# Performance work log

Hardware: AMD Instinct MI355X
Metric: run time of the kernel (lower is better)

The kernel has to match this reference:

```python
import jax, jax.numpy as jnp
import numpy as np

SEQ, BATCH, IN_DIM, HID = 1024, 512, 128, 128


def _linear_params(key, fan_in, fan_out):
    # matches torch nn.Linear default init: U(-1/sqrt(fan_in), 1/sqrt(fan_in))
    s = 1.0 / np.sqrt(fan_in)
    k1, k2 = jax.random.split(key)
    W = jax.random.uniform(k1, (fan_in, fan_out), minval=-s, maxval=s, dtype=jnp.float32)
    b = jax.random.uniform(k2, (fan_out,), minval=-s, maxval=s, dtype=jnp.float32)
    return W, b


def setup_inputs() -> dict:
    key = jax.random.key(0)
    ks = jax.random.split(key, 5)
    inputs = jax.random.normal(ks[0], (SEQ, BATCH, IN_DIM), dtype=jnp.float32)
    Wf, bf = _linear_params(ks[1], IN_DIM + HID, HID)
    Wi, bi = _linear_params(ks[2], IN_DIM + HID, HID)
    Wg, bg = _linear_params(ks[3], IN_DIM + HID, HID)
    Wo, bo = _linear_params(ks[4], IN_DIM + HID, HID)
    return {"inputs": inputs, "Wf": Wf, "bf": bf, "Wi": Wi, "bi": bi,
            "Wg": Wg, "bg": bg, "Wo": Wo, "bo": bo}


def reference(inputs, Wf, bf, Wi, bi, Wg, bg, Wo, bo):
    # inputs: [seq, batch, in_dim] (time-major, matches torch unbind(dim=0))
    B = inputs.shape[1]
    H = Wf.shape[1]
    h0 = jnp.zeros((B, H), dtype=inputs.dtype)
    c0 = jnp.zeros((B, H), dtype=inputs.dtype)

    def step(carry, x):
        hx, cx = carry
        comb = jnp.concatenate([x, hx], axis=1)  # [B, in_dim+H]
        f_lin = comb @ Wf + bf
        i_lin = comb @ Wi + bi
        g = jnp.tanh(comb @ Wg + bg)
        o = jax.nn.sigmoid(comb @ Wo + bo)
        # Quantum sampler, closed form:
        #  - RX(theta)|0> has <Z> = cos(theta)
        #  - CNOT chain over f-wires pulls Z_j back to Z_0...Z_j -> cumprod of cos
        #  - i-wires untouched by CNOTs -> plain cos
        #  probs = (<Z> + 1) / 2
        f = (jnp.cumprod(jnp.cos(f_lin), axis=1) + 1.0) * 0.5
        i = (jnp.cos(i_lin) + 1.0) * 0.5
        cx_new = f * cx + i * g
        hx_new = o * jnp.tanh(cx_new)
        return (hx_new, cx_new), hx_new

    (hx, cx), outputs = jax.lax.scan(step, (h0, c0), inputs)
    return outputs, hx, cx
```

## Files before the change

kernel.cpp:

```cpp
#include <hip/hip_runtime.h>

#define SEQ   1024
#define BATCH 512
#define HID   128

typedef __attribute__((ext_vector_type(8))) short  short8v;
typedef __attribute__((ext_vector_type(4))) float  float4v;
typedef __attribute__((ext_vector_type(2))) float  float2v;

__device__ __forceinline__ unsigned short f2bf(float f) {
    union { float f; unsigned u; } v; v.f = f;
    return (unsigned short)((v.u + 0x7fffu + ((v.u >> 16) & 1u)) >> 16);
}
__device__ __forceinline__ float fast_cos(float x) {
    return __builtin_amdgcn_cosf(x * 0.15915494309189535f);
}
__device__ __forceinline__ float fast_sigmoid(float x) {
    return __builtin_amdgcn_rcpf(1.0f + __builtin_amdgcn_exp2f(-1.4426950408889634f * x));
}
__device__ __forceinline__ float fast_tanh(float x) {
    return 1.0f - 2.0f * __builtin_amdgcn_rcpf(1.0f + __builtin_amdgcn_exp2f(2.8853900817779268f * x));
}
template<int CTRL, int RM>
__device__ __forceinline__ float dpp1(float v) {
    union { float f; int i; } s, o, r;
    s.f = v; o.f = 1.0f;
    r.i = __builtin_amdgcn_update_dpp(o.i, s.i, CTRL, RM, 0xf, false);
    return r.f;
}
#define BAR() do { asm volatile("s_waitcnt lgkmcnt(0)" ::: "memory");  \
                   __builtin_amdgcn_s_barrier();                       \
                   __builtin_amdgcn_sched_barrier(0); } while (0)

__global__ __launch_bounds__(512, 1) void qlstm_fused(
    const float* __restrict__ X,
    const float* __restrict__ Wf, const float* __restrict__ bfp,
    const float* __restrict__ Wi, const float* __restrict__ bip,
    const float* __restrict__ Wg, const float* __restrict__ bgp,
    const float* __restrict__ Wo, const float* __restrict__ bop,
    float* __restrict__ out)
{
    __shared__ alignas(16) float zring[8][4][HID][2];
    __shared__ alignas(16) float gact[2][4][HID];
    __shared__ alignas(8)  unsigned short h_bf[2][HID];
    __shared__ alignas(8)  unsigned short x_bf[2][HID];

    const int tid = threadIdx.x, lane = tid & 63, wid = tid >> 6;
    const int l15 = lane & 15, kg = lane >> 4;
    const int b0 = blockIdx.x * 2;
    const bool prod = (wid >= 4);
    const int g = wid & 3;
    const float* Wsel = (g == 0) ? Wf : (g == 1) ? Wi : (g == 2) ? Wg : Wo;
    const float* bsel = (g == 0) ? bfp : (g == 1) ? bip : (g == 2) ? bgp : bop;

    short8v bw[8][4];
    {
        const int kbase = prod ? 0 : 128;
        #pragma unroll
        for (int n = 0; n < 8; ++n) {
            const int col = n * 16 + l15;
            #pragma unroll
            for (int ks = 0; ks < 4; ++ks) {
                const int k0 = kbase + ks * 32 + kg * 8;
                short8v a;
                #pragma unroll
                for (int j = 0; j < 8; ++j)
                    a[j] = (short)f2bf(Wsel[(size_t)(k0 + j) * HID + col]);
                bw[n][ks] = a;
            }
        }
    }
    float biasr[8];
    #pragma unroll
    for (int n = 0; n < 8; ++n) biasr[n] = prod ? bsel[n * 16 + l15] : 0.f;

    if (tid < 128) ((unsigned*)h_bf)[tid] = 0u;

    const bool worker = !prod && ((wid >> 1) == (blockIdx.x & 1));
    const int wrow = wid & 1;
    float c0 = 0.f, c1 = 0.f, hL0 = 0.f, hL1 = 0.f;
    const int ca0 = kg * 32 + l15;

    #pragma unroll 1
    for (int p = 0; p < 4; ++p) {
        if (wid == 4) {
            float4v xv = *(const float4v*)(X + ((size_t)p * BATCH + b0) * HID + lane * 4);
            unsigned* dst = (unsigned*)&x_bf[lane >> 5][(lane & 31) * 4];
            dst[0] = (unsigned)f2bf(xv[0]) | ((unsigned)f2bf(xv[1]) << 16);
            dst[1] = (unsigned)f2bf(xv[2]) | ((unsigned)f2bf(xv[3]) << 16);
        }
        BAR();
        if (prod) {
            short8v ax[4];
            #pragma unroll
            for (int ks = 0; ks < 4; ++ks)
                ax[ks] = *(const short8v*)&x_bf[l15 & 1][ks * 32 + kg * 8];
            float4v acc[8];
            #pragma unroll
            for (int n = 0; n < 8; ++n)
                #pragma unroll
                for (int j = 0; j < 4; ++j) acc[n][j] = biasr[n];
            #pragma unroll
            for (int ks = 0; ks < 4; ++ks)
                #pragma unroll
                for (int n = 0; n < 8; ++n)
                    acc[n] = __builtin_amdgcn_mfma_f32_16x16x32_bf16(ax[ks], bw[n][ks], acc[n], 0, 0, 0);
            if (kg == 0) {
                #pragma unroll
                for (int n = 0; n < 8; ++n) {
                    float2v zz; zz[0] = acc[n][0]; zz[1] = acc[n][1];
                    *(float2v*)&zring[p][g][n * 16 + l15][0] = zz;
                }
            }
        }
        BAR();
    }

    float4v xv;
    if (wid == 4) xv = *(const float4v*)(X + ((size_t)4 * BATCH + b0) * HID + lane * 4);

    for (int t = 0; t < SEQ; ++t) {
        const int slot = t & 7;

        if (!prod) {
            short8v ah[4];
            #pragma unroll
            for (int ks = 0; ks < 4; ++ks)
                ah[ks] = *(const short8v*)&h_bf[l15 & 1][ks * 32 + kg * 8];

            float4v acc[8];
            #pragma unroll
            for (int n = 0; n < 8; ++n)
                #pragma unroll
                for (int j = 0; j < 4; ++j) acc[n][j] = 0.f;

            __builtin_amdgcn_s_setprio(1);
            #pragma unroll
            for (int ks = 0; ks < 4; ++ks)
                #pragma unroll
                for (int n = 0; n < 8; ++n)
                    acc[n] = __builtin_amdgcn_mfma_f32_16x16x32_bf16(ah[ks], bw[n][ks], acc[n], 0, 0, 0);
            __builtin_amdgcn_s_setprio(0);

            float2v zr0 = *(const float2v*)&zring[slot][g][ca0][0];
            float2v zr1 = *(const float2v*)&zring[slot][g][ca0 + 16][0];

            float s0r0 = (kg == 0) ? acc[0][0] : (kg == 1) ? acc[2][0]
                       : (kg == 2) ? acc[4][0] : acc[6][0];
            float s0r1 = (kg == 0) ? acc[0][1] : (kg == 1) ? acc[2][1]
                       : (kg == 2) ? acc[4][1] : acc[6][1];
            float s1r0 = (kg == 0) ? acc[1][0] : (kg == 1) ? acc[3][0]
                       : (kg == 2) ? acc[5][0] : acc[7][0];
            float s1r1 = (kg == 0) ? acc[1][1] : (kg == 1) ? acc[3][1]
                       : (kg == 2) ? acc[5][1] : acc[7][1];
            s0r0 += zr0[0]; s0r1 += zr0[1];
            s1r0 += zr1[0]; s1r1 += zr1[1];

            float v00, v01, v10, v11;
            if (g == 0) {
                v00 = fast_cos(s0r0); v01 = fast_cos(s1r0);
                v10 = fast_cos(s0r1); v11 = fast_cos(s1r1);
            } else if (g == 1) {
                v00 = (fast_cos(s0r0) + 1.f) * .5f; v01 = (fast_cos(s1r0) + 1.f) * .5f;
                v10 = (fast_cos(s0r1) + 1.f) * .5f; v11 = (fast_cos(s1r1) + 1.f) * .5f;
            } else if (g == 2) {
                v00 = fast_tanh(s0r0); v01 = fast_tanh(s1r0);
                v10 = fast_tanh(s0r1); v11 = fast_tanh(s1r1);
            } else {
                v00 = fast_sigmoid(s0r0); v01 = fast_sigmoid(s1r0);
                v10 = fast_sigmoid(s0r1); v11 = fast_sigmoid(s1r1);
            }
            gact[0][g][ca0]      = v00;
            gact[0][g][ca0 + 16] = v01;
            gact[1][g][ca0]      = v10;
            gact[1][g][ca0 + 16] = v11;
        } else if (wid == 4 && t + 4 < SEQ) {
            unsigned* dst = (unsigned*)&x_bf[lane >> 5][(lane & 31) * 4];
            dst[0] = (unsigned)f2bf(xv[0]) | ((unsigned)f2bf(xv[1]) << 16);
            dst[1] = (unsigned)f2bf(xv[2]) | ((unsigned)f2bf(xv[3]) << 16);
            if (t + 5 < SEQ)
                xv = *(const float4v*)(X + ((size_t)(t + 5) * BATCH + b0) * HID + lane * 4);
        }
        BAR();

        if (prod) {
            if (t + 4 < SEQ) {
                short8v ax[4];
                #pragma unroll
                for (int ks = 0; ks < 4; ++ks)
                    ax[ks] = *(const short8v*)&x_bf[l15 & 1][ks * 32 + kg * 8];
                float4v acc[8];
                #pragma unroll
                for (int n = 0; n < 8; ++n)
                    #pragma unroll
                    for (int j = 0; j < 4; ++j) acc[n][j] = biasr[n];
                __builtin_amdgcn_s_setprio(1);
                #pragma unroll
                for (int ks = 0; ks < 4; ++ks)
                    #pragma unroll
                    for (int n = 0; n < 8; ++n)
                        acc[n] = __builtin_amdgcn_mfma_f32_16x16x32_bf16(ax[ks], bw[n][ks], acc[n], 0, 0, 0);
                __builtin_amdgcn_s_setprio(0);
                if (kg == 0) {
                    const int sp = (t + 4) & 7;
                    #pragma unroll
                    for (int n = 0; n < 8; ++n) {
                        float2v zz; zz[0] = acc[n][0]; zz[1] = acc[n][1];
                        *(float2v*)&zring[sp][g][n * 16 + l15][0] = zz;
                    }
                }
            }
        } else if (worker) {
            float2v fc = *(const float2v*)&gact[wrow][0][2 * lane];
            float2v iv = *(const float2v*)&gact[wrow][1][2 * lane];
            float2v gv = *(const float2v*)&gact[wrow][2][2 * lane];
            float2v ov = *(const float2v*)&gact[wrow][3][2 * lane];

            const float pair = fc[0] * fc[1];
            float R = pair;
            R *= dpp1<0x111, 0xf>(R);
            R *= dpp1<0x112, 0xf>(R);
            R *= dpp1<0x114, 0xf>(R);
            R *= dpp1<0x118, 0xf>(R);
            const float Erow = dpp1<0x111, 0xf>(R);
            const float T0 = __shfl(R, 15);
            const float T1 = __shfl(R, 31);
            const float T2 = __shfl(R, 47);
            const float rp = (kg == 0) ? 1.f : (kg == 1) ? T0
                           : (kg == 2) ? T0 * T1 : T0 * T1 * T2;
            const float E  = Erow * rp;
            const float f0 = (E * fc[0] + 1.f) * 0.5f;
            const float f1 = (E * pair  + 1.f) * 0.5f;

            const float cn0 = fmaf(f0, c0, iv[0] * gv[0]);
            const float cn1 = fmaf(f1, c1, iv[1] * gv[1]);
            const float hn0 = ov[0] * fast_tanh(cn0);
            const float hn1 = ov[1] * fast_tanh(cn1);
            c0 = cn0; c1 = cn1; hL0 = hn0; hL1 = hn1;

            *(unsigned*)&h_bf[wrow][2 * lane] =
                (unsigned)f2bf(hn0) | ((unsigned)f2bf(hn1) << 16);
            float2v o2; o2[0] = hn0; o2[1] = hn1;
            *(float2v*)&out[((size_t)t * BATCH + b0 + wrow) * HID + 2 * lane] = o2;
        }
        BAR();
    }

    if (worker) {
        const size_t base = (size_t)SEQ * BATCH * HID;
        const size_t ro = (size_t)(b0 + wrow) * HID + 2 * lane;
        float2v h2, c2;
        h2[0] = hL0; h2[1] = hL1; c2[0] = c0; c2[1] = c1;
        *(float2v*)&out[base + ro] = h2;
        *(float2v*)&out[base + (size_t)BATCH * HID + ro] = c2;
    }
}

extern "C" void kernel_launch(void* const* d_in, const int* in_sizes, int n_in,
                              void* d_out, int out_size, void* d_ws, size_t ws_size,
                              hipStream_t stream) {
    const float* X  = (const float*)d_in[0];
    const float* Wf = (const float*)d_in[1];
    const float* bf = (const float*)d_in[2];
    const float* Wi = (const float*)d_in[3];
    const float* bi = (const float*)d_in[4];
    const float* Wg = (const float*)d_in[5];
    const float* bg = (const float*)d_in[6];
    const float* Wo = (const float*)d_in[7];
    const float* bo = (const float*)d_in[8];
    float* out = (float*)d_out;
    (void)d_ws; (void)ws_size;

    qlstm_fused<<<BATCH / 2, 512, 0, stream>>>(
        X, Wf, bf, Wi, bi, Wg, bg, Wo, bo, out);
}
```

Before: 1.209 ms.

## Move forget-gate cumprod scan into gate waves and spread cell update across all consumers

The cumulative product of cos over the forget gate moves out of the cell-update phase and into the gate-activation phase, where the wave computing the f-gate runs a DPP/shuffle scan and writes final probabilities. The cell update now runs on all four consumer waves, one element per lane, rather than on two waves handling two elements each. The x-projection producer work moves into the first phase alongside the recurrent matmul, and x staging shifts one step ahead. This shortens the serial second phase per timestep at the cost of a longer f-gate wave in the first phase. It also drops the setprio hints.

```diff
diff --git a/kernel.cpp b/kernel.cpp
--- a/kernel.cpp
+++ b/kernel.cpp
@@ -31,6 +31,24 @@
 #define BAR() do { asm volatile("s_waitcnt lgkmcnt(0)" ::: "memory");  \
                    __builtin_amdgcn_s_barrier();                       \
                    __builtin_amdgcn_sched_barrier(0); } while (0)
+
+__device__ __forceinline__ void fscan(float a, float b, int kg,
+                                      float& Fa, float& Fb) {
+    float Sa = a, Sb = b;
+    Sa *= dpp1<0x111, 0xf>(Sa);  Sb *= dpp1<0x111, 0xf>(Sb);
+    Sa *= dpp1<0x112, 0xf>(Sa);  Sb *= dpp1<0x112, 0xf>(Sb);
+    Sa *= dpp1<0x114, 0xf>(Sa);  Sb *= dpp1<0x114, 0xf>(Sb);
+    Sa *= dpp1<0x118, 0xf>(Sa);  Sb *= dpp1<0x118, 0xf>(Sb);
+    const float T0a = __shfl(Sa, 15), T0b = __shfl(Sb, 15);
+    const float T1a = __shfl(Sa, 31), T1b = __shfl(Sb, 31);
+    const float T2a = __shfl(Sa, 47), T2b = __shfl(Sb, 47);
+    const float Taown = __shfl(Sa, kg * 16 + 15);
+    const float p0 = T0a * T0b, p1 = T1a * T1b, p2 = T2a * T2b;
+    const float rp = (kg == 0) ? 1.f : (kg == 1) ? p0
+                   : (kg == 2) ? p0 * p1 : p0 * p1 * p2;
+    Fa = rp * Sa;
+    Fb = rp * Taown * Sb;
+}
 
 __global__ __launch_bounds__(512, 1) void qlstm_fused(
     const float* __restrict__ X,
@@ -76,18 +94,18 @@
 
     if (tid < 128) ((unsigned*)h_bf)[tid] = 0u;
 
-    const bool worker = !prod && ((wid >> 1) == (blockIdx.x & 1));
-    const int wrow = wid & 1;
-    float c0 = 0.f, c1 = 0.f, hL0 = 0.f, hL1 = 0.f;
+    const int crow = wid >> 1;
+    const int ccol = (wid & 1) * 64 + lane;
+    float c_reg = 0.f, h_last = 0.f;
     const int ca0 = kg * 32 + l15;
 
     #pragma unroll 1
     for (int p = 0; p < 4; ++p) {
         if (wid == 4) {
-            float4v xv = *(const float4v*)(X + ((size_t)p * BATCH + b0) * HID + lane * 4);
+            float4v xv0 = *(const float4v*)(X + ((size_t)p * BATCH + b0) * HID + lane * 4);
             unsigned* dst = (unsigned*)&x_bf[lane >> 5][(lane & 31) * 4];
-            dst[0] = (unsigned)f2bf(xv[0]) | ((unsigned)f2bf(xv[1]) << 16);
-            dst[1] = (unsigned)f2bf(xv[2]) | ((unsigned)f2bf(xv[3]) << 16);
+            dst[0] = (unsigned)f2bf(xv0[0]) | ((unsigned)f2bf(xv0[1]) << 16);
+            dst[1] = (unsigned)f2bf(xv0[2]) | ((unsigned)f2bf(xv0[3]) << 16);
         }
         BAR();
         if (prod) {
@@ -115,9 +133,15 @@
         }
         BAR();
     }
-
+    if (wid == 4) {
+        float4v xv0 = *(const float4v*)(X + ((size_t)4 * BATCH + b0) * HID + lane * 4);
+        unsigned* dst = (unsigned*)&x_bf[lane >> 5][(lane & 31) * 4];
+        dst[0] = (unsigned)f2bf(xv0[0]) | ((unsigned)f2bf(xv0[1]) << 16);
+        dst[1] = (unsigned)f2bf(xv0[2]) | ((unsigned)f2bf(xv0[3]) << 16);
+    }
+    BAR();
     float4v xv;
-    if (wid == 4) xv = *(const float4v*)(X + ((size_t)4 * BATCH + b0) * HID + lane * 4);
+    if (wid == 4) xv = *(const float4v*)(X + ((size_t)5 * BATCH + b0) * HID + lane * 4);
 
     for (int t = 0; t < SEQ; ++t) {
         const int slot = t & 7;
@@ -158,8 +182,11 @@
 
             float v00, v01, v10, v11;
             if (g == 0) {
-                v00 = fast_cos(s0r0); v01 = fast_cos(s1r0);
-                v10 = fast_cos(s0r1); v11 = fast_cos(s1r1);
+                float Fa0, Fb0, Fa1, Fb1;
+                fscan(fast_cos(s0r0), fast_cos(s1r0), kg, Fa0, Fb0);
+                fscan(fast_cos(s0r1), fast_cos(s1r1), kg, Fa1, Fb1);
+                v00 = (Fa0 + 1.f) * 0.5f; v01 = (Fb0 + 1.f) * 0.5f;
+                v10 = (Fa1 + 1.f) * 0.5f; v11 = (Fb1 + 1.f) * 0.5f;
             } else if (g == 1) {
                 v00 = (fast_cos(s0r0) + 1.f) * .5f; v01 = (fast_cos(s1r0) + 1.f) * .5f;
                 v10 = (fast_cos(s0r1) + 1.f) * .5f; v11 = (fast_cos(s1r1) + 1.f) * .5f;
@@ -174,85 +201,59 @@
             gact[0][g][ca0 + 16] = v01;
             gact[1][g][ca0]      = v10;
             gact[1][g][ca0 + 16] = v11;
-        } else if (wid == 4 && t + 4 < SEQ) {
-            unsigned* dst = (unsigned*)&x_bf[lane >> 5][(lane & 31) * 4];
-            dst[0] = (unsigned)f2bf(xv[0]) | ((unsigned)f2bf(xv[1]) << 16);
-            dst[1] = (unsigned)f2bf(xv[2]) | ((unsigned)f2bf(xv[3]) << 16);
-            if (t + 5 < SEQ)
-                xv = *(const float4v*)(X + ((size_t)(t + 5) * BATCH + b0) * HID + lane * 4);
-        }
-        BAR();
-
-        if (prod) {
-            if (t + 4 < SEQ) {
-                short8v ax[4];
-                #pragma unroll
-                for (int ks = 0; ks < 4; ++ks)
-                    ax[ks] = *(const short8v*)&x_bf[l15 & 1][ks * 32 + kg * 8];
-                float4v acc[8];
+        } else if (t + 4 < SEQ) {
+            short8v ax[4];
+            #pragma unroll
+            for (int ks = 0; ks < 4; ++ks)
+                ax[ks] = *(const short8v*)&x_bf[l15 & 1][ks * 32 + kg * 8];
+            float4v acc[8];
+            #pragma unroll
+            for (int n = 0; n < 8; ++n)
+                #pragma unroll
+                for (int j = 0; j < 4; ++j) acc[n][j] = biasr[n];
+            #pragma unroll
+            for (int ks = 0; ks < 4; ++ks)
                 #pragma unroll
                 for (int n = 0; n < 8; ++n)
-                    #pragma unroll
-                    for (int j = 0; j < 4; ++j) acc[n][j] = biasr[n];
-                __builtin_amdgcn_s_setprio(1);
-                #pragma unroll
-                for (int ks = 0; ks < 4; ++ks)
-                    #pragma unroll
-                    for (int n = 0; n < 8; ++n)
-                        acc[n] = __builtin_amdgcn_mfma_f32_16x16x32_bf16(ax[ks], bw[n][ks], acc[n], 0, 0, 0);
-                __builtin_amdgcn_s_setprio(0);
-                if (kg == 0) {
-                    const int sp = (t + 4) & 7;
-                    #pragma unroll
-                    for (int n = 0; n < 8; ++n) {
-                        float2v zz; zz[0] = acc[n][0]; zz[1] = acc[n][1];
-                        *(float2v*)&zring[sp][g][n * 16 + l15][0] = zz;
-                    }
+                    acc[n] = __builtin_amdgcn_mfma_f32_16x16x32_bf16(ax[ks], bw[n][ks], acc[n], 0, 0, 0);
+            if (kg == 0) {
+                const int sp = (t + 4) & 7;
+                #pragma unroll
+                for (int n = 0; n < 8; ++n) {
+                    float2v zz; zz[0] = acc[n][0]; zz[1] = acc[n][1];
+                    *(float2v*)&zring[sp][g][n * 16 + l15][0] = zz;
                 }
             }
-        } else if (worker) {
-            float2v fc = *(const float2v*)&gact[wrow][0][2 * lane];
-            float2v iv = *(const float2v*)&gact[wrow][1][2 * lane];
-            float2v gv = *(const float2v*)&gact[wrow][2][2 * lane];
-            float2v ov = *(const float2v*)&gact[wrow][3][2 * lane];
-
-            const float pair = fc[0] * fc[1];
-            float R = pair;
-            R *= dpp1<0x111, 0xf>(R);
-            R *= dpp1<0x112, 0xf>(R);
-            R *= dpp1<0x114, 0xf>(R);
-            R *= dpp1<0x118, 0xf>(R);
-            const float Erow = dpp1<0x111, 0xf>(R);
-            const float T0 = __shfl(R, 15);
-            const float T1 = __shfl(R, 31);
-            const float T2 = __shfl(R, 47);
-            const float rp = (kg == 0) ? 1.f : (kg == 1) ? T0
-                           : (kg == 2) ? T0 * T1 : T0 * T1 * T2;
-            const float E  = Erow * rp;
-            const float f0 = (E * fc[0] + 1.f) * 0.5f;
-            const float f1 = (E * pair  + 1.f) * 0.5f;
-
-            const float cn0 = fmaf(f0, c0, iv[0] * gv[0]);
-            const float cn1 = fmaf(f1, c1, iv[1] * gv[1]);
-            const float hn0 = ov[0] * fast_tanh(cn0);
-            const float hn1 = ov[1] * fast_tanh(cn1);
-            c0 = cn0; c1 = cn1; hL0 = hn0; hL1 = hn1;
-
-            *(unsigned*)&h_bf[wrow][2 * lane] =
-                (unsigned)f2bf(hn0) | ((unsigned)f2bf(hn1) << 16);
-            float2v o2; o2[0] = hn0; o2[1] = hn1;
-            *(float2v*)&out[((size_t)t * BATCH + b0 + wrow) * HID + 2 * lane] = o2;
-        }
-        BAR();
-    }
-
-    if (worker) {
+        }
+        BAR();
+
+        if (!prod) {
+            const float f  = gact[crow][0][ccol];
+            const float i_ = gact[crow][1][ccol];
+            const float g_ = gact[crow][2][ccol];
+            const float o_ = gact[crow][3][ccol];
+            const float cn = fmaf(f, c_reg, i_ * g_);
+            const float hn = o_ * fast_tanh(cn);
+            c_reg = cn; h_last = hn;
+            h_bf[crow][ccol] = f2bf(hn);
+            out[((size_t)t * BATCH + b0 + crow) * HID + ccol] = hn;
+        } else if (wid == 4) {
+            if (t + 5 < SEQ) {
+                unsigned* dst = (unsigned*)&x_bf[lane >> 5][(lane & 31) * 4];
+                dst[0] = (unsigned)f2bf(xv[0]) | ((unsigned)f2bf(xv[1]) << 16);
+                dst[1] = (unsigned)f2bf(xv[2]) | ((unsigned)f2bf(xv[3]) << 16);
+                if (t + 6 < SEQ)
+                    xv = *(const float4v*)(X + ((size_t)(t + 6) * BATCH + b0) * HID + lane * 4);
+            }
+        }
+        BAR();
+    }
+
+    if (!prod) {
         const size_t base = (size_t)SEQ * BATCH * HID;
-        const size_t ro = (size_t)(b0 + wrow) * HID + 2 * lane;
-        float2v h2, c2;
-        h2[0] = hL0; h2[1] = hL1; c2[0] = c0; c2[1] = c1;
-        *(float2v*)&out[base + ro] = h2;
-        *(float2v*)&out[base + (size_t)BATCH * HID + ro] = c2;
+        const size_t ro = (size_t)(b0 + crow) * HID + ccol;
+        out[base + ro] = h_last;
+        out[base + (size_t)BATCH * HID + ro] = c_reg;
     }
 }
 
```

Measured after the change: 1.111 ms. 1.09x faster.
